# Kernel tuning notes

Measured on AMD Instinct MI355X. Metric: run time of the kernel, lower is better.

## Reference

```python
import jax, jax.numpy as jnp
import numpy as np

H = 1024          # en_hidden_size
NUM_LAYERS = 3
NUM_CLASS = 60
IN_SIZE = 150
EPS = 1e-5


def _gru_dir(x, w_ih, w_hh, b_ih, b_hh):
    """Single-direction GRU run forward in time. x: [N,T,in] -> [N,T,H].
    PyTorch GRU cell math."""
    gi = jnp.einsum('nti,gi->ntg', x, w_ih) + b_ih  # [N,T,3H] input projections

    def step(h, gi_t):
        gh = h @ w_hh.T + b_hh
        i_r, i_z, i_n = jnp.split(gi_t, 3, axis=-1)
        h_r, h_z, h_n = jnp.split(gh, 3, axis=-1)
        r = jax.nn.sigmoid(i_r + h_r)
        z = jax.nn.sigmoid(i_z + h_z)
        n = jnp.tanh(i_n + r * h_n)
        h_new = (1.0 - z) * n + z * h
        return h_new, h_new

    h0 = jnp.zeros((x.shape[0], H), dtype=x.dtype)
    _, ys = jax.lax.scan(step, h0, jnp.swapaxes(gi, 0, 1))  # ys: [T,N,H]
    return jnp.swapaxes(ys, 0, 1)


def _bigru_forward(x, bn_gamma, bn_beta,
                   w_ih_0, w_hh_0, b_ih_0, b_hh_0,
                   w_ih_1, w_hh_1, b_ih_1, b_hh_1,
                   w_ih_2, w_hh_2, b_ih_2, b_hh_2,
                   fc_w, fc_b):
    # BatchNorm1d (train mode): stats over (N,T) per channel, biased variance.
    mean = jnp.mean(x, axis=(0, 1), keepdims=True)
    var = jnp.mean(jnp.square(x - mean), axis=(0, 1), keepdims=True)
    h_in = (x - mean) * jax.lax.rsqrt(var + EPS) * bn_gamma + bn_beta

    # NOTE: the original advances the bidirectional GRU one timestep at a time
    # while carrying the hidden state, so BOTH directions run forward in time.
    layer_params = [(w_ih_0, w_hh_0, b_ih_0, b_hh_0),
                    (w_ih_1, w_hh_1, b_ih_1, b_hh_1),
                    (w_ih_2, w_hh_2, b_ih_2, b_hh_2)]
    for (w_ih, w_hh, b_ih, b_hh) in layer_params:
        outs = [_gru_dir(h_in, w_ih[d], w_hh[d], b_ih[d], b_hh[d]) for d in range(2)]
        h_in = jnp.concatenate(outs, axis=-1)  # [N,T,2H]

    encoder_hidden = h_in                      # [N,T,2H]
    hidden = encoder_hidden[:, -1, :]          # seq_len == T for every sample
    out = hidden @ fc_w.T + fc_b               # [N, num_class]
    return out, encoder_hidden


def setup_inputs() -> dict:
    key = jax.random.key(0)
    ks = jax.random.split(key, 32)
    N, T = 256, 64
    s = 1.0 / np.sqrt(H)
    inp = {}
    inp['x'] = jax.random.normal(ks[0], (N, T, IN_SIZE), dtype=jnp.float32)
    inp['bn_gamma'] = jnp.ones((IN_SIZE,), jnp.float32)
    inp['bn_beta'] = jnp.zeros((IN_SIZE,), jnp.float32)
    in_sizes = [IN_SIZE, 2 * H, 2 * H]
    ki = 1
    for l in range(NUM_LAYERS):
        inp[f'w_ih_{l}'] = jax.random.uniform(ks[ki], (2, 3 * H, in_sizes[l]), jnp.float32, -s, s); ki += 1
        inp[f'w_hh_{l}'] = jax.random.uniform(ks[ki], (2, 3 * H, H), jnp.float32, -s, s); ki += 1
        inp[f'b_ih_{l}'] = jax.random.uniform(ks[ki], (2, 3 * H), jnp.float32, -s, s); ki += 1
        inp[f'b_hh_{l}'] = jax.random.uniform(ks[ki], (2, 3 * H), jnp.float32, -s, s); ki += 1
    inp['fc_w'] = jax.random.uniform(ks[ki], (NUM_CLASS, 2 * H), jnp.float32, -s, s); ki += 1
    inp['fc_b'] = jax.random.uniform(ks[ki], (NUM_CLASS,), jnp.float32, -s, s)
    return inp


def reference(x, bn_gamma, bn_beta,
              w_ih_0, w_hh_0, b_ih_0, b_hh_0,
              w_ih_1, w_hh_1, b_ih_1, b_hh_1,
              w_ih_2, w_hh_2, b_ih_2, b_hh_2,
              fc_w, fc_b):
    return _bigru_forward(x, bn_gamma, bn_beta,
                          w_ih_0, w_hh_0, b_ih_0, b_hh_0,
                          w_ih_1, w_hh_1, b_ih_1, b_hh_1,
                          w_ih_2, w_hh_2, b_ih_2, b_hh_2,
                          fc_w, fc_b)
```

## Files before the change

### kernel.cpp

```cpp
#include <hip/hip_runtime.h>
#include <hip/hip_bf16.h>
#include <math.h>

#define HH    1024
#define TT    64
#define NBAT  256
#define G3    3072
#define IN0   150
#define IN0P  160
#define NCLS  60
#define ENC_W 2048

typedef float  f32x4 __attribute__((ext_vector_type(4)));
typedef short  s16x8 __attribute__((ext_vector_type(8)));

#define GLOAD16(gsrc, ldst) \
  __builtin_amdgcn_global_load_lds((const __attribute__((address_space(1))) unsigned int*)(gsrc), \
                                   (__attribute__((address_space(3))) unsigned int*)(ldst), 16, 0, 0)

static __device__ inline short f2bf(float f) {
    __hip_bfloat16 h = __float2bfloat16(f);
    return *(short*)&h;
}

__global__ void bigru_bn_stats(const float* __restrict__ x,
                               float* __restrict__ mean, float* __restrict__ istd) {
    int f = blockIdx.x;
    int tid = threadIdx.x;
    double s = 0.0, s2 = 0.0;
    for (int i = tid; i < NBAT * TT; i += blockDim.x) {
        float v = x[(size_t)i * IN0 + f];
        s += v; s2 += (double)v * v;
    }
    __shared__ double sh[256], sh2[256];
    sh[tid] = s; sh2[tid] = s2;
    __syncthreads();
    for (int off = 128; off > 0; off >>= 1) {
        if (tid < off) { sh[tid] += sh[tid + off]; sh2[tid] += sh2[tid + off]; }
        __syncthreads();
    }
    if (tid == 0) {
        double m = sh[0] / (NBAT * TT);
        double var = sh2[0] / (NBAT * TT) - m * m;
        mean[f] = (float)m;
        istd[f] = (float)(1.0 / sqrt(var + 1e-5));
    }
}

__global__ void bigru_bn_apply_bf16(const float* __restrict__ x,
                                    const float* __restrict__ mean, const float* __restrict__ istd,
                                    const float* __restrict__ gamma, const float* __restrict__ beta,
                                    short* __restrict__ xn) {
    int idx = blockIdx.x * blockDim.x + threadIdx.x;
    if (idx >= NBAT * TT * IN0P) return;
    int f = idx % IN0P;
    int r = idx / IN0P;
    float v = 0.f;
    if (f < IN0) v = (x[(size_t)r * IN0 + f] - mean[f]) * istd[f] * gamma[f] + beta[f];
    xn[idx] = f2bf(v);
}

__global__ void bigru_cvt_wih0(const float* __restrict__ src, short* __restrict__ dst) {
    int idx = blockIdx.x * blockDim.x + threadIdx.x;
    if (idx >= 2 * G3 * IN0P) return;
    int f = idx % IN0P;
    int r = idx / IN0P;
    float v = (f < IN0) ? src[(size_t)r * IN0 + f] : 0.f;
    dst[idx] = f2bf(v);
}

__global__ void bigru_cvt4(const float* __restrict__ src, short* __restrict__ dst, int n4) {
    int i = blockIdx.x * blockDim.x + threadIdx.x;
    if (i >= n4) return;
    float4 v = ((const float4*)src)[i];
    short4 o;
    o.x = f2bf(v.x); o.y = f2bf(v.y); o.z = f2bf(v.z); o.w = f2bf(v.w);
    ((short4*)dst)[i] = o;
}

__global__ __launch_bounds__(256)
void bigru_gi_gemm(const short* __restrict__ Abase, int ldA, int K,
                   const short* __restrict__ W,
                   const float* __restrict__ b_ih,
                   float* __restrict__ gi,
                   int t0, int Mchunk) {
    int d    = blockIdx.z;
    int col0 = blockIdx.x * 128;
    int row0 = blockIdx.y * 128;

    __shared__ short As[128][32];
    __shared__ short Bs[128][32];

    int tid  = threadIdx.x;
    int lane = tid & 63;
    int w    = tid >> 6;
    int wm   = w & 1, wn = w >> 1;

    f32x4 acc[4][4];
    #pragma unroll
    for (int i = 0; i < 4; ++i)
        #pragma unroll
        for (int j = 0; j < 4; ++j)
            acc[i][j] = (f32x4){0.f, 0.f, 0.f, 0.f};

    const short* Wd = W + (size_t)d * G3 * K;
    int sr = lane >> 2;
    int sc = (lane & 3) * 8;

    for (int k0 = 0; k0 < K; k0 += 32) {
        #pragma unroll
        for (int q = 0; q < 2; ++q) {
            int r  = w * 32 + q * 16 + sr;
            int gr = row0 + r;
            int tt = gr >> 8, n = gr & 255;
            const short* ga = Abase + (size_t)(n * TT + t0 + tt) * ldA + k0 + sc;
            GLOAD16(ga, &As[w * 32 + q * 16][0]);
            const short* gb = Wd + (size_t)(col0 + r) * K + k0 + sc;
            GLOAD16(gb, &Bs[w * 32 + q * 16][0]);
        }
        __syncthreads();

        int fr = lane & 15, fq = (lane >> 4) * 8;
        s16x8 a[4], b[4];
        #pragma unroll
        for (int i = 0; i < 4; ++i) a[i] = *(const s16x8*)&As[wm * 64 + i * 16 + fr][fq];
        #pragma unroll
        for (int j = 0; j < 4; ++j) b[j] = *(const s16x8*)&Bs[wn * 64 + j * 16 + fr][fq];
        #pragma unroll
        for (int i = 0; i < 4; ++i)
            #pragma unroll
            for (int j = 0; j < 4; ++j)
                acc[i][j] = __builtin_amdgcn_mfma_f32_16x16x32_bf16(a[i], b[j], acc[i][j], 0, 0, 0);
        __syncthreads();
    }

    int fr = lane & 15, quad = lane >> 4;
    #pragma unroll
    for (int j = 0; j < 4; ++j) {
        int c = col0 + wn * 64 + j * 16 + fr;
        float bias = b_ih[d * G3 + c];
        #pragma unroll
        for (int i = 0; i < 4; ++i) {
            #pragma unroll
            for (int reg = 0; reg < 4; ++reg) {
                int r = row0 + wm * 64 + i * 16 + quad * 4 + reg;
                gi[((size_t)d * Mchunk + r) * G3 + c] = acc[i][j][reg] + bias;
            }
        }
    }
}

__global__ __launch_bounds__(512, 1)
void bigru_steps_fused(const short* __restrict__ w_hh,
                       const float* __restrict__ b_hh,
                       const float* __restrict__ gi,
                       float* __restrict__ h,
                       short* __restrict__ hbf,
                       float* __restrict__ enc,
                       short* __restrict__ enc_bf,
                       unsigned int* __restrict__ bar,
                       int t0, int Tc, int Mchunk) {
    __shared__ short Ws[48 * 1024];
    __shared__ short As[8][4][512];

    int b   = blockIdx.x;
    int d   = b & 1;
    int mt  = (b >> 1) & 1;
    int ct  = b >> 2;
    int grp = b & 3;

    int tid  = threadIdx.x;
    int lane = tid & 63;
    int w    = tid >> 6;
    int fr   = lane & 15;
    int quad = lane >> 4;
    int sw   = fr & 7;

    int j0 = ct * 16;
    int row_base = mt * 128 + w * 16;
    int jcol = j0 + fr;

    const short* Wd = w_hh + (size_t)d * G3 * HH;

    #pragma unroll
    for (int q = 0; q < 12; ++q) {
        int c  = w * 12 + q;
        int rr = c >> 1, kh = c & 1;
        int g  = rr >> 4, jc = rr & 15;
        const short* src = Wd + (size_t)(g * HH + j0 + jc) * HH
                         + (size_t)(kh * 64 + (lane ^ (rr & 7))) * 8;
        GLOAD16(src, &Ws[rr * 1024 + kh * 512]);
    }

    int l0 = lane & 1, l1 = (lane >> 1) & 1, l2 = (lane >> 2) & 1;
    int l3 = (lane >> 3) & 1, l4 = (lane >> 4) & 1, l5 = (lane >> 5) & 1;
    int arow = (l2 ^ l4) | (l3 << 1) | (l4 << 2) | (l5 << 3);
    int akb  = (l0 ^ l2 ^ l4) | ((l1 ^ l3) << 1);
    size_t a_src_off = (size_t)(row_base + arow) * HH + (size_t)akb * 8;

    float hreg[4];
    #pragma unroll
    for (int r = 0; r < 4; ++r) {
        int n = row_base + quad * 4 + r;
        hreg[r] = h[((size_t)d * NBAT + n) * HH + jcol];
    }
    float bhr = b_hh[d * G3 + jcol];
    float bhz = b_hh[d * G3 + HH + jcol];
    float bhn = b_hh[d * G3 + 2 * HH + jcol];

    __syncthreads();

    float gir[4], giz[4], gin[4];
    {
        size_t gb0 = ((size_t)d * Mchunk) * G3 + jcol;
        #pragma unroll
        for (int r = 0; r < 4; ++r) {
            int n = row_base + quad * 4 + r;
            size_t gg = gb0 + (size_t)n * G3;
            gir[r] = gi[gg];
            giz[r] = gi[gg + HH];
            gin[r] = gi[gg + 2 * HH];
        }
    }

    for (int tt = 0; tt < Tc; ++tt) {
        int t = t0 + tt;
        const short* hb = hbf + ((size_t)((t & 1) * 2 + d)) * NBAT * HH;
        short*       ho = hbf + ((size_t)(((t + 1) & 1) * 2 + d)) * NBAT * HH;
        const short* asrc = hb + a_src_off;

        f32x4 acc[3];
        #pragma unroll
        for (int g = 0; g < 3; ++g) acc[g] = (f32x4){0.f, 0.f, 0.f, 0.f};

        #pragma unroll
        for (int c = 0; c < 3; ++c)
            GLOAD16(asrc + c * 32, &As[w][c][0]);

        int rd_off = (fr * 64 + quad * 16) ^ ((fr & 7) << 4);

        #pragma unroll
        for (int c = 0; c < 32; ++c) {
            if (c < 30)       asm volatile("s_waitcnt vmcnt(2)");
            else if (c == 30) asm volatile("s_waitcnt vmcnt(1)");
            else              asm volatile("s_waitcnt vmcnt(0)");
            __builtin_amdgcn_sched_barrier(0);
            s16x8 a = *(const s16x8*)((const char*)&As[w][c & 3][0] + rd_off);
            int ks = c * 4 + quad;
            #pragma unroll
            for (int g = 0; g < 3; ++g) {
                s16x8 bg = *(const s16x8*)&Ws[(g * 16 + fr) * 1024 + ((ks ^ sw) << 3)];
                acc[g] = __builtin_amdgcn_mfma_f32_16x16x32_bf16(a, bg, acc[g], 0, 0, 0);
            }
            __builtin_amdgcn_sched_barrier(0);
            if (c + 3 < 32)
                GLOAD16(asrc + (c + 3) * 32, &As[w][(c + 3) & 3][0]);
        }

        #pragma unroll
        for (int r = 0; r < 4; ++r) {
            int n = row_base + quad * 4 + r;
            float hrv = acc[0][r] + bhr;
            float hzv = acc[1][r] + bhz;
            float hnv = acc[2][r] + bhn;
            float rg = 1.f / (1.f + __expf(-(gir[r] + hrv)));
            float zg = 1.f / (1.f + __expf(-(giz[r] + hzv)));
            float ng = tanhf(gin[r] + rg * hnv);
            float hnew = (1.f - zg) * ng + zg * hreg[r];
            hreg[r] = hnew;
            ho[(size_t)n * HH + jcol] = f2bf(hnew);
            size_t eidx = ((size_t)n * TT + t) * ENC_W + (size_t)d * HH + jcol;
            if (enc_bf) enc_bf[eidx] = f2bf(hnew);
            if (enc)    enc[eidx]    = hnew;
        }

        if (tt == Tc - 1) {
            #pragma unroll
            for (int r = 0; r < 4; ++r) {
                int n = row_base + quad * 4 + r;
                h[((size_t)d * NBAT + n) * HH + jcol] = hreg[r];
            }
        } else {
            size_t gbn = ((size_t)d * Mchunk + (size_t)(tt + 1) * NBAT) * G3 + jcol;
            #pragma unroll
            for (int r = 0; r < 4; ++r) {
                int n = row_base + quad * 4 + r;
                size_t gg = gbn + (size_t)n * G3;
                gir[r] = gi[gg];
                giz[r] = gi[gg + HH];
                gin[r] = gi[gg + 2 * HH];
            }
            __syncthreads();
            if (tid == 0) {
                unsigned int* c = &bar[grp * 32];
                __hip_atomic_fetch_add(c, 1u, __ATOMIC_RELEASE, __HIP_MEMORY_SCOPE_AGENT);
                unsigned tgt = 64u * (unsigned)(tt + 1);
                while (__hip_atomic_load(c, __ATOMIC_ACQUIRE, __HIP_MEMORY_SCOPE_AGENT) < tgt)
                    __builtin_amdgcn_s_sleep(2);
            }
            __syncthreads();
        }
    }
}

__global__ void bigru_fc(const float* __restrict__ enc, const float* __restrict__ fc_w,
                         const float* __restrict__ fc_b, float* __restrict__ out) {
    int n = blockIdx.x;
    int tid = threadIdx.x;
    __shared__ float hbuf[ENC_W];
    for (int k = tid; k < ENC_W; k += blockDim.x)
        hbuf[k] = enc[(size_t)n * TT * ENC_W + (size_t)(TT - 1) * ENC_W + k];
    __syncthreads();
    if (tid < NCLS) {
        float acc = fc_b[tid];
        for (int k = 0; k < ENC_W; ++k)
            acc += hbuf[k] * fc_w[(size_t)tid * ENC_W + k];
        out[(size_t)n * NCLS + tid] = acc;
    }
}

extern "C" void kernel_launch(void* const* d_in, const int* in_sizes, int n_in,
                              void* d_out, int out_size, void* d_ws, size_t ws_size,
                              hipStream_t stream) {
    const float* x        = (const float*)d_in[0];
    const float* bn_gamma = (const float*)d_in[1];
    const float* bn_beta  = (const float*)d_in[2];
    const float* w_ih[3]  = {(const float*)d_in[3], (const float*)d_in[7],  (const float*)d_in[11]};
    const float* w_hh[3]  = {(const float*)d_in[4], (const float*)d_in[8],  (const float*)d_in[12]};
    const float* b_ih[3]  = {(const float*)d_in[5], (const float*)d_in[9],  (const float*)d_in[13]};
    const float* b_hh[3]  = {(const float*)d_in[6], (const float*)d_in[10], (const float*)d_in[14]};
    const float* fc_w     = (const float*)d_in[15];
    const float* fc_b     = (const float*)d_in[16];

    float* out = (float*)d_out;
    float* enc = out + NBAT * NCLS;

    char* base = (char*)d_ws;
    size_t off = 0;
    auto alloc = [&](size_t bytes) {
        void* p = base + off;
        off += (bytes + 255) & ~(size_t)255;
        return p;
    };
    float* mean      = (float*)alloc(IN0 * 4);
    float* istd      = (float*)alloc(IN0 * 4);
    short* xn_bf     = (short*)alloc((size_t)NBAT * TT * IN0P * 2);
    short* wih0_bf   = (short*)alloc((size_t)2 * G3 * IN0P * 2);
    short* wih_bf    = (short*)alloc((size_t)2 * G3 * ENC_W * 2);
    short* whh_bf    = (short*)alloc((size_t)2 * G3 * HH * 2);
    float* h         = (float*)alloc((size_t)2 * NBAT * HH * 4);
    short* hbf       = (short*)alloc((size_t)2 * 2 * NBAT * HH * 2);
    short* enc_bf    = (short*)alloc((size_t)NBAT * TT * ENC_W * 2);
    unsigned int* bar = (unsigned int*)alloc(4 * 32 * sizeof(unsigned int));
    size_t fixed = off;

    int Tc = 1;
    for (int cand : {16, 8, 4, 2, 1}) {
        size_t gi_bytes = (size_t)2 * NBAT * cand * G3 * 4;
        if (fixed + gi_bytes + 1024 <= ws_size) { Tc = cand; break; }
    }
    float* gi = (float*)alloc((size_t)2 * NBAT * Tc * G3 * 4);
    int Mchunk = NBAT * Tc;

    bigru_bn_stats<<<IN0, 256, 0, stream>>>(x, mean, istd);
    bigru_bn_apply_bf16<<<(NBAT * TT * IN0P + 255) / 256, 256, 0, stream>>>(
        x, mean, istd, bn_gamma, bn_beta, xn_bf);

    bigru_cvt_wih0<<<(2 * G3 * IN0P + 255) / 256, 256, 0, stream>>>(w_ih[0], wih0_bf);

    for (int l = 0; l < 3; ++l) {
        if (l > 0) {
            int n4 = (2 * G3 * ENC_W) / 4;
            bigru_cvt4<<<(n4 + 255) / 256, 256, 0, stream>>>(w_ih[l], wih_bf, n4);
        }
        {
            int n4 = (2 * G3 * HH) / 4;
            bigru_cvt4<<<(n4 + 255) / 256, 256, 0, stream>>>(w_hh[l], whh_bf, n4);
        }
        hipMemsetAsync(h, 0, (size_t)2 * NBAT * HH * 4, stream);
        hipMemsetAsync(hbf, 0, (size_t)2 * 2 * NBAT * HH * 2, stream);

        const short* Abase = (l == 0) ? xn_bf : enc_bf;
        int ldA = (l == 0) ? IN0P : ENC_W;
        int K   = (l == 0) ? IN0P : ENC_W;
        const short* W = (l == 0) ? wih0_bf : wih_bf;

        for (int t0 = 0; t0 < TT; t0 += Tc) {
            bigru_gi_gemm<<<dim3(G3 / 128, Mchunk / 128, 2), 256, 0, stream>>>(
                Abase, ldA, K, W, b_ih[l], gi, t0, Mchunk);

            hipMemsetAsync(bar, 0, 4 * 32 * sizeof(unsigned int), stream);

            const short* whh_c   = whh_bf;
            const float* bhh_c   = b_hh[l];
            const float* gi_c    = gi;
            float*       h_c     = h;
            short*       hbf_c   = hbf;
            float*       enc_c   = (l == 2) ? enc : nullptr;
            short*       encbf_c = (l == 2) ? nullptr : enc_bf;
            unsigned int* bar_c  = bar;
            int a_t0 = t0, a_tc = Tc, a_mc = Mchunk;
            void* kargs[] = { &whh_c, &bhh_c, &gi_c, &h_c, &hbf_c,
                              &enc_c, &encbf_c, &bar_c, &a_t0, &a_tc, &a_mc };
            hipLaunchCooperativeKernel((const void*)bigru_steps_fused,
                                       dim3(256), dim3(512), kargs, 0, stream);
        }
    }

    bigru_fc<<<NBAT, 256, 0, stream>>>(enc, fc_w, fc_b, out);
}
```

Before: 4.835 ms.

## Replace atomic-counter barrier with per-block flags and load A operand directly to registers

The per-group grid barrier changes from a single atomic counter that every block increments and spins on to per-block flag slots. Each block stores its step number in its own padded slot, and one wavefront polls all 64 flags in parallel using a wave vote. The recurrent hidden-state A operand no longer goes through LDS via async global-to-LDS loads. Each lane instead prefetches 16-byte vectors straight into a 32-entry register array, 12 chunks ahead. Launch bounds change to allow two blocks per CU. Atomic contention and LDS staging go away, at the cost of much higher register pressure and possible spills.

```diff
diff --git a/kernel.cpp b/kernel.cpp
--- a/kernel.cpp
+++ b/kernel.cpp
@@ -150,7 +150,7 @@
     }
 }
 
-__global__ __launch_bounds__(512, 1)
+__global__ __launch_bounds__(512, 2)
 void bigru_steps_fused(const short* __restrict__ w_hh,
                        const float* __restrict__ b_hh,
                        const float* __restrict__ gi,
@@ -161,7 +161,6 @@
                        unsigned int* __restrict__ bar,
                        int t0, int Tc, int Mchunk) {
     __shared__ short Ws[48 * 1024];
-    __shared__ short As[8][4][512];
 
     int b   = blockIdx.x;
     int d   = b & 1;
@@ -192,12 +191,6 @@
         GLOAD16(src, &Ws[rr * 1024 + kh * 512]);
     }
 
-    int l0 = lane & 1, l1 = (lane >> 1) & 1, l2 = (lane >> 2) & 1;
-    int l3 = (lane >> 3) & 1, l4 = (lane >> 4) & 1, l5 = (lane >> 5) & 1;
-    int arow = (l2 ^ l4) | (l3 << 1) | (l4 << 2) | (l5 << 3);
-    int akb  = (l0 ^ l2 ^ l4) | ((l1 ^ l3) << 1);
-    size_t a_src_off = (size_t)(row_base + arow) * HH + (size_t)akb * 8;
-
     float hreg[4];
     #pragma unroll
     for (int r = 0; r < 4; ++r) {
@@ -207,6 +200,8 @@
     float bhr = b_hh[d * G3 + jcol];
     float bhz = b_hh[d * G3 + HH + jcol];
     float bhn = b_hh[d * G3 + 2 * HH + jcol];
+
+    size_t a_src_off = (size_t)(row_base + fr) * HH + (size_t)quad * 8;
 
     __syncthreads();
 
@@ -233,28 +228,22 @@
         #pragma unroll
         for (int g = 0; g < 3; ++g) acc[g] = (f32x4){0.f, 0.f, 0.f, 0.f};
 
-        #pragma unroll
-        for (int c = 0; c < 3; ++c)
-            GLOAD16(asrc + c * 32, &As[w][c][0]);
-
-        int rd_off = (fr * 64 + quad * 16) ^ ((fr & 7) << 4);
+        s16x8 areg[32];
+        #pragma unroll
+        for (int c = 0; c < 12; ++c)
+            areg[c] = *(const s16x8*)(asrc + c * 32);
 
         #pragma unroll
         for (int c = 0; c < 32; ++c) {
-            if (c < 30)       asm volatile("s_waitcnt vmcnt(2)");
-            else if (c == 30) asm volatile("s_waitcnt vmcnt(1)");
-            else              asm volatile("s_waitcnt vmcnt(0)");
-            __builtin_amdgcn_sched_barrier(0);
-            s16x8 a = *(const s16x8*)((const char*)&As[w][c & 3][0] + rd_off);
+            if (c + 12 < 32)
+                areg[c + 12] = *(const s16x8*)(asrc + (c + 12) * 32);
+            s16x8 a = areg[c];
             int ks = c * 4 + quad;
             #pragma unroll
             for (int g = 0; g < 3; ++g) {
                 s16x8 bg = *(const s16x8*)&Ws[(g * 16 + fr) * 1024 + ((ks ^ sw) << 3)];
                 acc[g] = __builtin_amdgcn_mfma_f32_16x16x32_bf16(a, bg, acc[g], 0, 0, 0);
             }
-            __builtin_amdgcn_sched_barrier(0);
-            if (c + 3 < 32)
-                GLOAD16(asrc + (c + 3) * 32, &As[w][(c + 3) & 3][0]);
         }
 
         #pragma unroll
@@ -291,12 +280,20 @@
                 gin[r] = gi[gg + 2 * HH];
             }
             __syncthreads();
-            if (tid == 0) {
-                unsigned int* c = &bar[grp * 32];
-                __hip_atomic_fetch_add(c, 1u, __ATOMIC_RELEASE, __HIP_MEMORY_SCOPE_AGENT);
-                unsigned tgt = 64u * (unsigned)(tt + 1);
-                while (__hip_atomic_load(c, __ATOMIC_ACQUIRE, __HIP_MEMORY_SCOPE_AGENT) < tgt)
-                    __builtin_amdgcn_s_sleep(2);
+            if (w == 0) {
+                unsigned int* fl = bar + (size_t)grp * 64 * 16;
+                __threadfence();
+                if (lane == 0)
+                    __hip_atomic_store(&fl[ct * 16], (unsigned)(tt + 1),
+                                       __ATOMIC_RELAXED, __HIP_MEMORY_SCOPE_AGENT);
+                unsigned tgt = (unsigned)(tt + 1);
+                for (;;) {
+                    unsigned v = __hip_atomic_load(&fl[lane * 16],
+                                                   __ATOMIC_ACQUIRE, __HIP_MEMORY_SCOPE_AGENT);
+                    if (__all(v >= tgt)) break;
+                    __builtin_amdgcn_s_sleep(4);
+                }
+                __threadfence();
             }
             __syncthreads();
         }
@@ -351,7 +348,7 @@
     float* h         = (float*)alloc((size_t)2 * NBAT * HH * 4);
     short* hbf       = (short*)alloc((size_t)2 * 2 * NBAT * HH * 2);
     short* enc_bf    = (short*)alloc((size_t)NBAT * TT * ENC_W * 2);
-    unsigned int* bar = (unsigned int*)alloc(4 * 32 * sizeof(unsigned int));
+    unsigned int* bar = (unsigned int*)alloc((size_t)4 * 64 * 16 * sizeof(unsigned int));
     size_t fixed = off;
 
     int Tc = 1;
@@ -389,7 +386,7 @@
             bigru_gi_gemm<<<dim3(G3 / 128, Mchunk / 128, 2), 256, 0, stream>>>(
                 Abase, ldA, K, W, b_ih[l], gi, t0, Mchunk);
 
-            hipMemsetAsync(bar, 0, 4 * 32 * sizeof(unsigned int), stream);
+            hipMemsetAsync(bar, 0, (size_t)4 * 64 * 16 * sizeof(unsigned int), stream);
 
             const short* whh_c   = whh_bf;
             const float* bhh_c   = b_hh[l];
```

Result: slower. 7.042 ms (+45.6%).
